# Kernel optimization log

Measured on AMD Instinct MI355X. Metric: run time of the kernel, lower is better.

The kernel has to match this reference:

```python
import jax, jax.numpy as jnp
import numpy as np

B, N, C = 4, 1024, 768
H, K, TEMP = 12, 32, 1.0
D = C // H
EPS = 1e-9


def setup_inputs() -> dict:
    key = jax.random.key(0)
    ks = jax.random.split(key, 5)
    x = jax.random.normal(ks[0], (B, N, C), dtype=jnp.float32)
    u = jax.random.uniform(ks[1], (B, N, N), dtype=jnp.float32)
    qkv_w = jax.random.normal(ks[2], (C, 3 * C), dtype=jnp.float32) * 0.02
    qkv_b = jnp.zeros((3 * C,), dtype=jnp.float32)
    proj_w = jax.random.normal(ks[3], (C, C), dtype=jnp.float32) * 0.02
    proj_b = jnp.zeros((C,), dtype=jnp.float32)
    head_scores = jnp.ones((H,), dtype=jnp.float32)
    return {"x": x, "u": u, "qkv_w": qkv_w, "qkv_b": qkv_b,
            "proj_w": proj_w, "proj_b": proj_b, "head_scores": head_scores}


def reference(x, u, qkv_w, qkv_b, proj_w, proj_b, head_scores):
    # qkv projection: [B,N,3C] -> [3,B,H,N,D]
    qkv = (x @ qkv_w + qkv_b).reshape(B, N, 3, H, D)
    qkv = jnp.transpose(qkv, (2, 0, 3, 1, 4))
    q, k, v = qkv[0], qkv[1], qkv[2]

    scale = 1.0 / np.sqrt(D)
    # full dense scores [B,H,N,N] (torch computes this twice; same math once)
    scores = jnp.einsum('bhnd,bhmd->bhnm', q, k) * scale

    # Gumbel top-K gate over head-averaged logits
    logits = scores.mean(axis=1)                         # [B,N,N]
    gumbel = -jnp.log(-jnp.log(u + EPS) + EPS)
    probs = jax.nn.softmax((logits + gumbel) / TEMP, axis=-1)
    topk_vals = jax.lax.top_k(probs, K)[0]               # sorted descending
    thresh = topk_vals[..., -1:]                          # K-th largest
    sparse_mask = (probs >= thresh).astype(scores.dtype)  # [B,N,N]

    # post-softmax masking (breaks flash fusion)
    attn = jax.nn.softmax(scores, axis=-1) * sparse_mask[:, None]
    out = jnp.einsum('bhnm,bhmd->bhnd', attn, v)          # [B,H,N,D]
    out = jnp.transpose(out, (0, 2, 1, 3)).reshape(B, N, C)
    return (out * head_scores.mean()) @ proj_w + proj_b
```

## Files before the change

kernel.cpp:

```cpp
#include <hip/hip_runtime.h>
#include <hip/hip_bf16.h>
#include <math.h>

#define B_ 4
#define N_ 1024
#define C_ 768
#define H_ 12
#define D_ 64
#define TOPK_ 32
#define EPS_ 1e-9f

#define LDN_ 32
#define LK_  72
#define QKS_ 1536

typedef __attribute__((ext_vector_type(8))) short bf16x8;
typedef __attribute__((ext_vector_type(4))) float f32x4;
typedef unsigned short u16;

struct TopkRec { unsigned int cnt; unsigned short c[62]; };

__device__ __forceinline__ u16 f2bf(float f) {
    unsigned int u = __float_as_uint(f);
    u += 0x7fffu + ((u >> 16) & 1u);
    return (u16)(u >> 16);
}
__device__ __forceinline__ float bf2f(u16 h) {
    return __uint_as_float(((unsigned int)h) << 16);
}

__device__ __forceinline__ void gll16(const void* g, void* l) {
    __builtin_amdgcn_global_load_lds(
        (const __attribute__((address_space(1))) void*)g,
        (__attribute__((address_space(3))) void*)l, 16, 0, 0);
}

__global__ __launch_bounds__(256) void conv_x(
    const float* __restrict__ X, u16* __restrict__ Xh, u16* __restrict__ Xl)
{
    const size_t off = ((size_t)blockIdx.x * 256 + threadIdx.x) * 8;
    float4 a = *(const float4*)&X[off];
    float4 b = *(const float4*)&X[off + 4];
    float v[8] = {a.x, a.y, a.z, a.w, b.x, b.y, b.z, b.w};
    u16 hb[8], lb[8];
    #pragma unroll
    for (int i = 0; i < 8; ++i) {
        u16 hi = f2bf(v[i]);
        hb[i] = hi;
        lb[i] = f2bf(v[i] - bf2f(hi));
    }
    *(bf16x8*)&Xh[off] = *(const bf16x8*)&hb[0];
    *(bf16x8*)&Xl[off] = *(const bf16x8*)&lb[0];
}

__global__ __launch_bounds__(256) void conv_w_nt(
    const float* __restrict__ W, u16* __restrict__ Wt_h, u16* __restrict__ Wt_l,
    int Kdim, int Ncols)
{
    __shared__ float Ts[64][65];
    const int t  = threadIdx.x;
    const int r  = t >> 2;
    const int cq = (t & 3) * 16;
    const int n0 = blockIdx.x * 64, k0 = blockIdx.y * 64;

    #pragma unroll
    for (int q = 0; q < 4; ++q) {
        float4 v = *(const float4*)&W[(size_t)(k0 + r) * Ncols + n0 + cq + q * 4];
        Ts[r][cq + q * 4 + 0] = v.x;
        Ts[r][cq + q * 4 + 1] = v.y;
        Ts[r][cq + q * 4 + 2] = v.z;
        Ts[r][cq + q * 4 + 3] = v.w;
    }
    __syncthreads();
    u16 hb[16], lb[16];
    #pragma unroll
    for (int i = 0; i < 16; ++i) {
        float val = Ts[cq + i][r];
        u16 hi = f2bf(val);
        hb[i] = hi;
        lb[i] = f2bf(val - bf2f(hi));
    }
    const size_t obase = (size_t)(n0 + r) * Kdim + k0 + cq;
    *(bf16x8*)&Wt_h[obase]     = *(const bf16x8*)&hb[0];
    *(bf16x8*)&Wt_h[obase + 8] = *(const bf16x8*)&hb[8];
    *(bf16x8*)&Wt_l[obase]     = *(const bf16x8*)&lb[0];
    *(bf16x8*)&Wt_l[obase + 8] = *(const bf16x8*)&lb[8];
}

__global__ __launch_bounds__(256) void gemm_qkv(
    const u16* __restrict__ Ath, const u16* __restrict__ Atl,
    const u16* __restrict__ Bth, const u16* __restrict__ Btl,
    const float* __restrict__ bias,
    u16* __restrict__ Ch, u16* __restrict__ Cl, float* __restrict__ Vf)
{
    __shared__ __align__(16) char smem[34816];
    u16* Ah = (u16*)(smem);
    u16* Al = (u16*)(smem + 8192);
    u16* Bh = (u16*)(smem + 16384);
    u16* Bl = (u16*)(smem + 24576);

    const int t    = threadIdx.x;
    const int d    = blockIdx.x;
    const int xcd  = d & 7, j = d >> 3;
    const int xt   = (xcd & 1) * 9 + (j % 9);
    const int yt   = (xcd >> 1) * 8 + (j / 9);
    const int m0   = yt * 128, n0 = xt * 128;
    const int lane = t & 63, w = t >> 6;
    const int wm   = (w >> 1) * 64, wn = (w & 1) * 64;
    const int fr   = lane & 15, kg8 = lane >> 4;
    const int w16  = w * 16;
    const int r4s  = lane >> 2, q4s = (lane & 3) * 8;

    f32x4 acc[4][4];
    #pragma unroll
    for (int i = 0; i < 4; ++i)
        #pragma unroll
        for (int j2 = 0; j2 < 4; ++j2)
            acc[i][j2] = (f32x4){0.f, 0.f, 0.f, 0.f};

    for (int kt = 0; kt < 24; ++kt) {
        const int k0 = kt * 32;
        __syncthreads();
        {
            const size_t ga0 = (size_t)(m0 + w16 + r4s) * C_ + k0 + q4s;
            const size_t ga1 = ga0 + (size_t)64 * C_;
            const size_t gb0 = (size_t)(n0 + w16 + r4s) * C_ + k0 + q4s;
            const size_t gb1 = gb0 + (size_t)64 * C_;
            gll16(&Ath[ga0], &Ah[w16 * LDN_]);
            gll16(&Ath[ga1], &Ah[(64 + w16) * LDN_]);
            gll16(&Atl[ga0], &Al[w16 * LDN_]);
            gll16(&Atl[ga1], &Al[(64 + w16) * LDN_]);
            gll16(&Bth[gb0], &Bh[w16 * LDN_]);
            gll16(&Bth[gb1], &Bh[(64 + w16) * LDN_]);
            gll16(&Btl[gb0], &Bl[w16 * LDN_]);
            gll16(&Btl[gb1], &Bl[(64 + w16) * LDN_]);
        }
        __syncthreads();

        bf16x8 aF[4], bF[4], a2F[4], b2F[4];
        #pragma unroll
        for (int fm = 0; fm < 4; ++fm)
            aF[fm] = *(const bf16x8*)&Ah[(wm + fm * 16 + fr) * LDN_ + kg8 * 8];
        #pragma unroll
        for (int fn = 0; fn < 4; ++fn)
            bF[fn] = *(const bf16x8*)&Bh[(wn + fn * 16 + fr) * LDN_ + kg8 * 8];
        #pragma unroll
        for (int fm = 0; fm < 4; ++fm)
            #pragma unroll
            for (int fn = 0; fn < 4; ++fn)
                acc[fm][fn] = __builtin_amdgcn_mfma_f32_16x16x32_bf16(
                    aF[fm], bF[fn], acc[fm][fn], 0, 0, 0);
        #pragma unroll
        for (int fn = 0; fn < 4; ++fn)
            b2F[fn] = *(const bf16x8*)&Bl[(wn + fn * 16 + fr) * LDN_ + kg8 * 8];
        #pragma unroll
        for (int fm = 0; fm < 4; ++fm)
            #pragma unroll
            for (int fn = 0; fn < 4; ++fn)
                acc[fm][fn] = __builtin_amdgcn_mfma_f32_16x16x32_bf16(
                    aF[fm], b2F[fn], acc[fm][fn], 0, 0, 0);
        #pragma unroll
        for (int fm = 0; fm < 4; ++fm)
            a2F[fm] = *(const bf16x8*)&Al[(wm + fm * 16 + fr) * LDN_ + kg8 * 8];
        #pragma unroll
        for (int fm = 0; fm < 4; ++fm)
            #pragma unroll
            for (int fn = 0; fn < 4; ++fn)
                acc[fm][fn] = __builtin_amdgcn_mfma_f32_16x16x32_bf16(
                    a2F[fm], bF[fn], acc[fm][fn], 0, 0, 0);
    }
    __syncthreads();

    const bool isV = (n0 >= 1536);
    float* Ts = (float*)(smem + w * 8448);
    const int lr8 = lane >> 3, lc8 = (lane & 7) * 8;
    #pragma unroll
    for (int p = 0; p < 2; ++p) {
        #pragma unroll
        for (int fmh = 0; fmh < 2; ++fmh) {
            const int fm = p * 2 + fmh;
            #pragma unroll
            for (int fn = 0; fn < 4; ++fn) {
                const float bv = bias[n0 + wn + fn * 16 + fr];
                #pragma unroll
                for (int i = 0; i < 4; ++i)
                    Ts[(fmh * 16 + kg8 * 4 + i) * 66 + fn * 16 + fr] =
                        acc[fm][fn][i] + bv;
            }
        }
        #pragma unroll
        for (int it = 0; it < 4; ++it) {
            const int r = it * 8 + lr8;
            float v[8];
            #pragma unroll
            for (int c = 0; c < 8; ++c) v[c] = Ts[r * 66 + lc8 + c];
            const int grow = m0 + wm + p * 32 + r;
            const int gcol = n0 + wn + lc8;
            if (isV) {
                float4 v0 = {v[0], v[1], v[2], v[3]};
                float4 v1 = {v[4], v[5], v[6], v[7]};
                float* vp = &Vf[(size_t)grow * C_ + gcol - 1536];
                *(float4*)vp       = v0;
                *(float4*)(vp + 4) = v1;
            } else {
                u16 hb[8], lb[8];
                #pragma unroll
                for (int c = 0; c < 8; ++c) {
                    u16 hi = f2bf(v[c]);
                    hb[c] = hi;
                    lb[c] = f2bf(v[c] - bf2f(hi));
                }
                *(bf16x8*)&Ch[(size_t)grow * QKS_ + gcol] = *(const bf16x8*)&hb[0];
                *(bf16x8*)&Cl[(size_t)grow * QKS_ + gcol] = *(const bf16x8*)&lb[0];
            }
        }
    }
}

__global__ __launch_bounds__(256) void attn_fused(
    const u16* __restrict__ qh, const u16* __restrict__ ql,
    const float* __restrict__ u, float* __restrict__ z,
    float2* __restrict__ mlp)
{
    __shared__ u16 KsH[128 * LK_], KsL[128 * LK_];

    const int t    = threadIdx.x;
    const int lane = t & 63, w = t >> 6;
    const int fr   = lane & 15, kg8 = lane >> 4;
    const int n0   = blockIdx.x * 64;
    const int m0   = blockIdx.y * 128;
    const int mc   = blockIdx.y;
    const int b    = blockIdx.z;

    f32x4 zacc[8];
    #pragma unroll
    for (int fn = 0; fn < 8; ++fn) zacc[fn] = (f32x4){0.f, 0.f, 0.f, 0.f};

    const int skr = t >> 1, skd = (t & 1) * 32;

    bf16x8 kAr[8], kBr[8], qAr[4], qBr[4];

    auto loadK = [&](bf16x8 (&kr)[8], int hd) {
        const size_t kb = (size_t)(b * N_ + m0 + skr) * QKS_ + 768 + hd * 64 + skd;
        kr[0] = *(const bf16x8*)&qh[kb];
        kr[1] = *(const bf16x8*)&qh[kb + 8];
        kr[2] = *(const bf16x8*)&qh[kb + 16];
        kr[3] = *(const bf16x8*)&qh[kb + 24];
        kr[4] = *(const bf16x8*)&ql[kb];
        kr[5] = *(const bf16x8*)&ql[kb + 8];
        kr[6] = *(const bf16x8*)&ql[kb + 16];
        kr[7] = *(const bf16x8*)&ql[kb + 24];
    };
    auto loadQ = [&](bf16x8 (&qr)[4], int hd) {
        const size_t qb = (size_t)(b * N_ + n0 + w * 16 + fr) * QKS_ + hd * 64 + kg8 * 8;
        qr[0] = *(const bf16x8*)&qh[qb];
        qr[1] = *(const bf16x8*)&qh[qb + 32];
        qr[2] = *(const bf16x8*)&ql[qb];
        qr[3] = *(const bf16x8*)&ql[qb + 32];
    };
    auto writeK = [&](const bf16x8 (&kr)[8]) {
        const int sb = skr * LK_ + skd;
        *(bf16x8*)&KsH[sb]      = kr[0];  *(bf16x8*)&KsH[sb + 8]  = kr[1];
        *(bf16x8*)&KsH[sb + 16] = kr[2];  *(bf16x8*)&KsH[sb + 24] = kr[3];
        *(bf16x8*)&KsL[sb]      = kr[4];  *(bf16x8*)&KsL[sb + 8]  = kr[5];
        *(bf16x8*)&KsL[sb + 16] = kr[6];  *(bf16x8*)&KsL[sb + 24] = kr[7];
    };
    auto compute = [&](const bf16x8 (&qr)[4], int hd) {
        f32x4 acc[8];
        #pragma unroll
        for (int fn = 0; fn < 8; ++fn) acc[fn] = (f32x4){0.f, 0.f, 0.f, 0.f};
        #pragma unroll
        for (int fn = 0; fn < 8; ++fn) {
            const int bidx = (fn * 16 + fr) * LK_ + kg8 * 8;
            bf16x8 bH = *(const bf16x8*)&KsH[bidx];
            bf16x8 bL = *(const bf16x8*)&KsL[bidx];
            acc[fn] = __builtin_amdgcn_mfma_f32_16x16x32_bf16(qr[0], bH, acc[fn], 0, 0, 0);
            acc[fn] = __builtin_amdgcn_mfma_f32_16x16x32_bf16(qr[0], bL, acc[fn], 0, 0, 0);
            acc[fn] = __builtin_amdgcn_mfma_f32_16x16x32_bf16(qr[2], bH, acc[fn], 0, 0, 0);
        }
        #pragma unroll
        for (int fn = 0; fn < 8; ++fn) {
            const int bidx = (fn * 16 + fr) * LK_ + 32 + kg8 * 8;
            bf16x8 bH = *(const bf16x8*)&KsH[bidx];
            bf16x8 bL = *(const bf16x8*)&KsL[bidx];
            acc[fn] = __builtin_amdgcn_mfma_f32_16x16x32_bf16(qr[1], bH, acc[fn], 0, 0, 0);
            acc[fn] = __builtin_amdgcn_mfma_f32_16x16x32_bf16(qr[1], bL, acc[fn], 0, 0, 0);
            acc[fn] = __builtin_amdgcn_mfma_f32_16x16x32_bf16(qr[3], bH, acc[fn], 0, 0, 0);
        }
        #pragma unroll
        for (int fn = 0; fn < 8; ++fn) {
            zacc[fn][0] += acc[fn][0];
            zacc[fn][1] += acc[fn][1];
            zacc[fn][2] += acc[fn][2];
            zacc[fn][3] += acc[fn][3];
        }
        #pragma unroll
        for (int reg = 0; reg < 4; ++reg) {
            float tmax = acc[0][reg];
            #pragma unroll
            for (int fn = 1; fn < 8; ++fn) tmax = fmaxf(tmax, acc[fn][reg]);
            tmax *= 0.125f;
            tmax = fmaxf(tmax, __shfl_xor(tmax, 1));
            tmax = fmaxf(tmax, __shfl_xor(tmax, 2));
            tmax = fmaxf(tmax, __shfl_xor(tmax, 4));
            tmax = fmaxf(tmax, __shfl_xor(tmax, 8));
            float tsum = 0.f;
            #pragma unroll
            for (int fn = 0; fn < 8; ++fn)
                tsum += expf(acc[fn][reg] * 0.125f - tmax);
            tsum += __shfl_xor(tsum, 1);
            tsum += __shfl_xor(tsum, 2);
            tsum += __shfl_xor(tsum, 4);
            tsum += __shfl_xor(tsum, 8);
            if (fr == 0) {
                const int n = n0 + w * 16 + kg8 * 4 + reg;
                mlp[(((size_t)(b * H_ + hd)) * N_ + n) * 8 + mc] =
                    make_float2(tmax, tsum);
            }
        }
    };

    loadQ(qAr, 0);
    loadK(kAr, 0);
    for (int hp = 0; hp < 6; ++hp) {
        const int hd0 = hp * 2, hd1 = hp * 2 + 1;
        __syncthreads();
        writeK(kAr);
        __syncthreads();
        loadQ(qBr, hd1);
        loadK(kBr, hd1);
        compute(qAr, hd0);
        __syncthreads();
        writeK(kBr);
        __syncthreads();
        if (hp < 5) {
            loadQ(qAr, hd0 + 2);
            loadK(kAr, hd0 + 2);
        }
        compute(qBr, hd1);
    }

    const float sc = 0.125f / 12.0f;
    #pragma unroll
    for (int fn = 0; fn < 8; ++fn) {
        const int m = m0 + fn * 16 + fr;
        #pragma unroll
        for (int reg = 0; reg < 4; ++reg) {
            const int n = n0 + w * 16 + kg8 * 4 + reg;
            const float uv = u[((size_t)(b * N_ + n)) * N_ + m];
            const float g  = -logf(-logf(uv + EPS_) + EPS_);
            z[((size_t)(b * N_ + n)) * N_ + m] = zacc[fn][reg] * sc + g;
        }
    }
}

__global__ __launch_bounds__(256) void ml_merge(
    const float2* __restrict__ mlp, float2* __restrict__ ml)
{
    const size_t idx = (size_t)blockIdx.x * 256 + threadIdx.x;
    float2 p[8];
    #pragma unroll
    for (int i = 0; i < 8; ++i) p[i] = mlp[idx * 8 + i];
    float m = p[0].x;
    #pragma unroll
    for (int i = 1; i < 8; ++i) m = fmaxf(m, p[i].x);
    float l = 0.f;
    #pragma unroll
    for (int i = 0; i < 8; ++i) l += p[i].y * expf(p[i].x - m);
    ml[idx] = make_float2(m, l);
}

__global__ __launch_bounds__(64) void topk_cols_kernel(
    const float* __restrict__ z, TopkRec* __restrict__ recs)
{
    const int row  = blockIdx.x;
    const int lane = threadIdx.x;
    const float* zr = z + (size_t)row * N_;
    float zv[16], wk[16];
    #pragma unroll
    for (int j = 0; j < 16; ++j) { zv[j] = zr[lane + 64 * j]; wk[j] = zv[j]; }

    float thresh = -INFINITY;
    for (int it = 0; it < TOPK_; ++it) {
        float lm = wk[0]; int li = 0;
        #pragma unroll
        for (int j = 1; j < 16; ++j)
            if (wk[j] > lm) { lm = wk[j]; li = j; }
        float gm = lm;
        gm = fmaxf(gm, __shfl_xor(gm, 1));
        gm = fmaxf(gm, __shfl_xor(gm, 2));
        gm = fmaxf(gm, __shfl_xor(gm, 4));
        gm = fmaxf(gm, __shfl_xor(gm, 8));
        gm = fmaxf(gm, __shfl_xor(gm, 16));
        gm = fmaxf(gm, __shfl_xor(gm, 32));
        unsigned long long has = __ballot(lm == gm);
        int first = __ffsll((unsigned long long)has) - 1;
        if (lane == first) wk[li] = -INFINITY;
        thresh = gm;
    }

    const unsigned long long below = ((unsigned long long)1 << lane) - 1;
    unsigned int basec = 0;
    TopkRec* rec = recs + row;
    #pragma unroll
    for (int j = 0; j < 16; ++j) {
        unsigned long long wmask = __ballot(zv[j] >= thresh);
        if (zv[j] >= thresh) {
            unsigned int pos = basec + (unsigned int)__popcll(wmask & below);
            if (pos < 62u) rec->c[pos] = (unsigned short)(lane + 64 * j);
        }
        basec += (unsigned int)__popcll(wmask);
    }
    if (lane == 0) rec->cnt = basec > 62u ? 62u : basec;
}

__global__ __launch_bounds__(256) void sparse_pv_kernel(
    const u16* __restrict__ qh, const u16* __restrict__ ql,
    const float* __restrict__ Vf,
    const TopkRec* __restrict__ recs, const float2* __restrict__ ml,
    const float* __restrict__ head_scores,
    u16* __restrict__ out1h, u16* __restrict__ out1l)
{
    __shared__ int cols_s[62];
    __shared__ int cnt_s;

    const int t    = threadIdx.x;
    const int lane = t & 63, wv = t >> 6;
    const int c4   = lane >> 2;
    const int dq   = lane & 3;
    const int row  = blockIdx.x;
    const int b    = row >> 10, n = row & 1023;

    const TopkRec* rec = recs + row;
    if (t == 0) cnt_s = (int)min(rec->cnt, 62u);
    if (t < 62) cols_s[t] = rec->c[t];

    float hsum = 0.f;
    #pragma unroll
    for (int i = 0; i < H_; ++i) hsum += head_scores[i];
    const float hs_mean = hsum * (1.0f / 12.0f);
    __syncthreads();
    const int cnt = cnt_s;
    const int nbatch = (cnt + 15) >> 4;

    for (int hd = wv; hd < H_; hd += 4) {
        float qv[16];
        {
            const size_t qb = (size_t)row * QKS_ + hd * 64 + dq * 16;
            bf16x8 qh0 = *(const bf16x8*)&qh[qb], qh1 = *(const bf16x8*)&qh[qb + 8];
            bf16x8 ql0 = *(const bf16x8*)&ql[qb], ql1 = *(const bf16x8*)&ql[qb + 8];
            #pragma unroll
            for (int i = 0; i < 8; ++i) {
                qv[i]     = bf2f((u16)qh0[i]) + bf2f((u16)ql0[i]);
                qv[i + 8] = bf2f((u16)qh1[i]) + bf2f((u16)ql1[i]);
            }
        }
        const float2 mlv = ml[((size_t)(b * H_ + hd)) * N_ + n];

        float acc[16];
        #pragma unroll
        for (int i = 0; i < 16; ++i) acc[i] = 0.f;

        for (int batch = 0; batch < nbatch; ++batch) {
            const int cidx  = batch * 16 + c4;
            const bool valid = (cidx < cnt);
            const int col   = cols_s[valid ? cidx : cnt - 1];

            const size_t kb = (size_t)(b * N_ + col) * QKS_ + 768 + hd * 64 + dq * 16;
            bf16x8 kh0 = *(const bf16x8*)&qh[kb], kh1 = *(const bf16x8*)&qh[kb + 8];
            bf16x8 kl0 = *(const bf16x8*)&ql[kb], kl1 = *(const bf16x8*)&ql[kb + 8];
            float dot = 0.f;
            #pragma unroll
            for (int i = 0; i < 8; ++i) {
                dot += qv[i]     * (bf2f((u16)kh0[i]) + bf2f((u16)kl0[i]));
                dot += qv[i + 8] * (bf2f((u16)kh1[i]) + bf2f((u16)kl1[i]));
            }
            dot += __shfl_xor(dot, 1);
            dot += __shfl_xor(dot, 2);
            float p = valid ? expf(dot * 0.125f - mlv.x) : 0.f;

            const float* vb = &Vf[(size_t)(b * N_ + col) * C_ + hd * 64 + dq * 16];
            #pragma unroll
            for (int q = 0; q < 4; ++q) {
                float4 v4 = *(const float4*)&vb[q * 4];
                acc[q * 4 + 0] += p * v4.x;
                acc[q * 4 + 1] += p * v4.y;
                acc[q * 4 + 2] += p * v4.z;
                acc[q * 4 + 3] += p * v4.w;
            }
        }

        #pragma unroll
        for (int d = 4; d < 64; d <<= 1)
            #pragma unroll
            for (int i = 0; i < 16; ++i)
                acc[i] += __shfl_xor(acc[i], d);

        if (c4 == 0) {
            const float s = hs_mean / mlv.y;
            u16 hb[16], lb[16];
            #pragma unroll
            for (int i = 0; i < 16; ++i) {
                float val = acc[i] * s;
                u16 hi = f2bf(val);
                hb[i] = hi;
                lb[i] = f2bf(val - bf2f(hi));
            }
            const size_t ob = (size_t)row * C_ + hd * 64 + dq * 16;
            *(bf16x8*)&out1h[ob]     = *(const bf16x8*)&hb[0];
            *(bf16x8*)&out1h[ob + 8] = *(const bf16x8*)&hb[8];
            *(bf16x8*)&out1l[ob]     = *(const bf16x8*)&lb[0];
            *(bf16x8*)&out1l[ob + 8] = *(const bf16x8*)&lb[8];
        }
    }
}

__global__ __launch_bounds__(256) void gemm_proj(
    const u16* __restrict__ Ath, const u16* __restrict__ Atl,
    const u16* __restrict__ Bth, const u16* __restrict__ Btl,
    const float* __restrict__ bias, float* __restrict__ Cm)
{
    __shared__ __align__(16) char smem[33792];
    u16* Ah = (u16*)(smem);
    u16* Al = (u16*)(smem + 4096);
    u16* Bh = (u16*)(smem + 8192);
    u16* Bl = (u16*)(smem + 16384);

    const int t    = threadIdx.x;
    const int d    = blockIdx.x;
    const int xcd  = d & 7, j = d >> 3;
    const int xt   = j % 6;
    const int yt   = xcd * 8 + j / 6;
    const int m0   = yt * 64, n0 = xt * 128;
    const int lane = t & 63, w = t >> 6;
    const int wm   = (w & 1) * 32, wn = (w >> 1) * 64;
    const int fr   = lane & 15, kg8 = lane >> 4;
    const int w16  = w * 16;
    const int r4s  = lane >> 2, q4s = (lane & 3) * 8;

    f32x4 acc[2][4];
    #pragma unroll
    for (int i = 0; i < 2; ++i)
        #pragma unroll
        for (int j2 = 0; j2 < 4; ++j2)
            acc[i][j2] = (f32x4){0.f, 0.f, 0.f, 0.f};

    for (int kt = 0; kt < 24; ++kt) {
        const int k0 = kt * 32;
        __syncthreads();
        {
            const size_t ga  = (size_t)(m0 + w16 + r4s) * C_ + k0 + q4s;
            const size_t gb0 = (size_t)(n0 + w * 32 + r4s) * C_ + k0 + q4s;
            const size_t gb1 = gb0 + (size_t)16 * C_;
            gll16(&Ath[ga],  &Ah[w16 * LDN_]);
            gll16(&Atl[ga],  &Al[w16 * LDN_]);
            gll16(&Bth[gb0], &Bh[(w * 32) * LDN_]);
            gll16(&Bth[gb1], &Bh[(w * 32 + 16) * LDN_]);
            gll16(&Btl[gb0], &Bl[(w * 32) * LDN_]);
            gll16(&Btl[gb1], &Bl[(w * 32 + 16) * LDN_]);
        }
        __syncthreads();

        bf16x8 aF[2], bF[4], a2F[2], b2F[4];
        #pragma unroll
        for (int fm = 0; fm < 2; ++fm)
            aF[fm] = *(const bf16x8*)&Ah[(wm + fm * 16 + fr) * LDN_ + kg8 * 8];
        #pragma unroll
        for (int fn = 0; fn < 4; ++fn)
            bF[fn] = *(const bf16x8*)&Bh[(wn + fn * 16 + fr) * LDN_ + kg8 * 8];
        #pragma unroll
        for (int fm = 0; fm < 2; ++fm)
            #pragma unroll
            for (int fn = 0; fn < 4; ++fn)
                acc[fm][fn] = __builtin_amdgcn_mfma_f32_16x16x32_bf16(
                    aF[fm], bF[fn], acc[fm][fn], 0, 0, 0);
        #pragma unroll
        for (int fn = 0; fn < 4; ++fn)
            b2F[fn] = *(const bf16x8*)&Bl[(wn + fn * 16 + fr) * LDN_ + kg8 * 8];
        #pragma unroll
        for (int fm = 0; fm < 2; ++fm)
            #pragma unroll
            for (int fn = 0; fn < 4; ++fn)
                acc[fm][fn] = __builtin_amdgcn_mfma_f32_16x16x32_bf16(
                    aF[fm], b2F[fn], acc[fm][fn], 0, 0, 0);
        #pragma unroll
        for (int fm = 0; fm < 2; ++fm)
            a2F[fm] = *(const bf16x8*)&Al[(wm + fm * 16 + fr) * LDN_ + kg8 * 8];
        #pragma unroll
        for (int fm = 0; fm < 2; ++fm)
            #pragma unroll
            for (int fn = 0; fn < 4; ++fn)
                acc[fm][fn] = __builtin_amdgcn_mfma_f32_16x16x32_bf16(
                    a2F[fm], bF[fn], acc[fm][fn], 0, 0, 0);
    }
    __syncthreads();

    float* Ts = (float*)(smem + w * 8448);
    const int lr8 = lane >> 3, lc8 = (lane & 7) * 8;
    #pragma unroll
    for (int fm = 0; fm < 2; ++fm)
        #pragma unroll
        for (int fn = 0; fn < 4; ++fn) {
            const float bv = bias[n0 + wn + fn * 16 + fr];
            #pragma unroll
            for (int i = 0; i < 4; ++i)
                Ts[(fm * 16 + kg8 * 4 + i) * 66 + fn * 16 + fr] =
                    acc[fm][fn][i] + bv;
        }
    #pragma unroll
    for (int it = 0; it < 4; ++it) {
        const int r = it * 8 + lr8;
        float v[8];
        #pragma unroll
        for (int c = 0; c < 8; ++c) v[c] = Ts[r * 66 + lc8 + c];
        const int grow = m0 + wm + r;
        const int gcol = n0 + wn + lc8;
        float4 v0 = {v[0], v[1], v[2], v[3]};
        float4 v1 = {v[4], v[5], v[6], v[7]};
        float* cp = &Cm[(size_t)grow * C_ + gcol];
        *(float4*)cp       = v0;
        *(float4*)(cp + 4) = v1;
    }
}

extern "C" void kernel_launch(void* const* d_in, const int* in_sizes, int n_in,
                              void* d_out, int out_size, void* d_ws, size_t ws_size,
                              hipStream_t stream)
{
    (void)in_sizes; (void)n_in; (void)out_size; (void)ws_size;
    const float* x           = (const float*)d_in[0];
    const float* u           = (const float*)d_in[1];
    const float* qkv_w       = (const float*)d_in[2];
    const float* qkv_b       = (const float*)d_in[3];
    const float* proj_w      = (const float*)d_in[4];
    const float* proj_b      = (const float*)d_in[5];
    const float* head_scores = (const float*)d_in[6];
    float* out = (float*)d_out;

    char* ws = (char*)d_ws;
    u16*     qkv_h  = (u16*)ws;
    u16*     qkv_l  = (u16*)(ws + 12582912);
    float*   Vf     = (float*)(ws + 25165824);
    char*    R      = ws + 37748736;
    u16*     wq_t_h = (u16*)R;
    u16*     wq_t_l = (u16*)(R + 3538944);
    float*   z      = (float*)R;
    TopkRec* recs   = (TopkRec*)(R + 16777216);
    u16*     wp_t_h = (u16*)R;
    u16*     wp_t_l = (u16*)(R + 1179648);
    float2*  ml     = (float2*)(R + 2359296);
    u16*     out1h  = (u16*)(R + 2752512);
    u16*     out1l  = (u16*)(R + 9043968);
    u16*     x_h    = (u16*)d_out;
    u16*     x_l    = (u16*)((char*)d_out + 6291456);
    float2*  mlp    = (float2*)d_out;

    conv_x<<<dim3(4096 * 768 / 8 / 256), dim3(256), 0, stream>>>(x, x_h, x_l);

    conv_w_nt<<<dim3(2304 / 64, 768 / 64), dim3(256), 0, stream>>>(
        qkv_w, wq_t_h, wq_t_l, 768, 2304);

    gemm_qkv<<<dim3(576), dim3(256), 0, stream>>>(
        x_h, x_l, wq_t_h, wq_t_l, qkv_b, qkv_h, qkv_l, Vf);

    attn_fused<<<dim3(16, 8, B_), dim3(256), 0, stream>>>(
        qkv_h, qkv_l, u, z, mlp);

    topk_cols_kernel<<<dim3(B_ * N_), dim3(64), 0, stream>>>(z, recs);

    conv_w_nt<<<dim3(768 / 64, 768 / 64), dim3(256), 0, stream>>>(
        proj_w, wp_t_h, wp_t_l, 768, 768);

    ml_merge<<<dim3(B_ * H_ * N_ / 256), dim3(256), 0, stream>>>(mlp, ml);

    sparse_pv_kernel<<<dim3(B_ * N_), dim3(256), 0, stream>>>(
        qkv_h, qkv_l, Vf, recs, ml, head_scores, out1h, out1l);

    gemm_proj<<<dim3(384), dim3(256), 0, stream>>>(
        out1h, out1l, wp_t_h, wp_t_l, proj_b, out);
}
```

Before: 269.5 us.

## Double-buffer LDS tiles in QKV and projection GEMMs to overlap loads

Both split-bf16 GEMM kernels now use two LDS buffers and prefetch the next K-tile with global-to-LDS loads while the current tile feeds the MFMAs. Partial vmcnt waits and raw barriers replace the two __syncthreads per iteration, so global latency is meant to be hidden behind compute. LDS use roughly doubles (64KB and 48KB per block), which can lower occupancy.

```diff
diff --git a/kernel.cpp b/kernel.cpp
--- a/kernel.cpp
+++ b/kernel.cpp
@@ -93,11 +93,7 @@
     const float* __restrict__ bias,
     u16* __restrict__ Ch, u16* __restrict__ Cl, float* __restrict__ Vf)
 {
-    __shared__ __align__(16) char smem[34816];
-    u16* Ah = (u16*)(smem);
-    u16* Al = (u16*)(smem + 8192);
-    u16* Bh = (u16*)(smem + 16384);
-    u16* Bl = (u16*)(smem + 24576);
+    __shared__ __align__(16) char smem[65536];
 
     const int t    = threadIdx.x;
     const int d    = blockIdx.x;
@@ -111,6 +107,26 @@
     const int w16  = w * 16;
     const int r4s  = lane >> 2, q4s = (lane & 3) * 8;
 
+    auto stage = [&](int k0, int buf) {
+        char* base = smem + buf * 32768;
+        u16* Ah = (u16*)(base);
+        u16* Al = (u16*)(base + 8192);
+        u16* Bh = (u16*)(base + 16384);
+        u16* Bl = (u16*)(base + 24576);
+        const size_t ga0 = (size_t)(m0 + w16 + r4s) * C_ + k0 + q4s;
+        const size_t ga1 = ga0 + (size_t)64 * C_;
+        const size_t gb0 = (size_t)(n0 + w16 + r4s) * C_ + k0 + q4s;
+        const size_t gb1 = gb0 + (size_t)64 * C_;
+        gll16(&Ath[ga0], &Ah[w16 * LDN_]);
+        gll16(&Ath[ga1], &Ah[(64 + w16) * LDN_]);
+        gll16(&Atl[ga0], &Al[w16 * LDN_]);
+        gll16(&Atl[ga1], &Al[(64 + w16) * LDN_]);
+        gll16(&Bth[gb0], &Bh[w16 * LDN_]);
+        gll16(&Bth[gb1], &Bh[(64 + w16) * LDN_]);
+        gll16(&Btl[gb0], &Bl[w16 * LDN_]);
+        gll16(&Btl[gb1], &Bl[(64 + w16) * LDN_]);
+    };
+
     f32x4 acc[4][4];
     #pragma unroll
     for (int i = 0; i < 4; ++i)
@@ -118,24 +134,25 @@
         for (int j2 = 0; j2 < 4; ++j2)
             acc[i][j2] = (f32x4){0.f, 0.f, 0.f, 0.f};
 
+    stage(0, 0);
     for (int kt = 0; kt < 24; ++kt) {
-        const int k0 = kt * 32;
-        __syncthreads();
-        {
-            const size_t ga0 = (size_t)(m0 + w16 + r4s) * C_ + k0 + q4s;
-            const size_t ga1 = ga0 + (size_t)64 * C_;
-            const size_t gb0 = (size_t)(n0 + w16 + r4s) * C_ + k0 + q4s;
-            const size_t gb1 = gb0 + (size_t)64 * C_;
-            gll16(&Ath[ga0], &Ah[w16 * LDN_]);
-            gll16(&Ath[ga1], &Ah[(64 + w16) * LDN_]);
-            gll16(&Atl[ga0], &Al[w16 * LDN_]);
-            gll16(&Atl[ga1], &Al[(64 + w16) * LDN_]);
-            gll16(&Bth[gb0], &Bh[w16 * LDN_]);
-            gll16(&Bth[gb1], &Bh[(64 + w16) * LDN_]);
-            gll16(&Btl[gb0], &Bl[w16 * LDN_]);
-            gll16(&Btl[gb1], &Bl[(64 + w16) * LDN_]);
-        }
-        __syncthreads();
+        if (kt < 23) {
+            asm volatile("s_waitcnt lgkmcnt(0)" ::: "memory");
+            __builtin_amdgcn_s_barrier();
+            __builtin_amdgcn_sched_barrier(0);
+            stage((kt + 1) * 32, (kt + 1) & 1);
+            asm volatile("s_waitcnt vmcnt(8)" ::: "memory");
+        } else {
+            asm volatile("s_waitcnt vmcnt(0)" ::: "memory");
+        }
+        __builtin_amdgcn_s_barrier();
+        __builtin_amdgcn_sched_barrier(0);
+
+        char* base = smem + (kt & 1) * 32768;
+        u16* Ah = (u16*)(base);
+        u16* Al = (u16*)(base + 8192);
+        u16* Bh = (u16*)(base + 16384);
+        u16* Bl = (u16*)(base + 24576);
 
         bf16x8 aF[4], bF[4], a2F[4], b2F[4];
         #pragma unroll
@@ -520,11 +537,7 @@
     const u16* __restrict__ Bth, const u16* __restrict__ Btl,
     const float* __restrict__ bias, float* __restrict__ Cm)
 {
-    __shared__ __align__(16) char smem[33792];
-    u16* Ah = (u16*)(smem);
-    u16* Al = (u16*)(smem + 4096);
-    u16* Bh = (u16*)(smem + 8192);
-    u16* Bl = (u16*)(smem + 16384);
+    __shared__ __align__(16) char smem[49152];
 
     const int t    = threadIdx.x;
     const int d    = blockIdx.x;
@@ -538,6 +551,23 @@
     const int w16  = w * 16;
     const int r4s  = lane >> 2, q4s = (lane & 3) * 8;
 
+    auto stage = [&](int k0, int buf) {
+        char* base = smem + buf * 24576;
+        u16* Ah = (u16*)(base);
+        u16* Al = (u16*)(base + 4096);
+        u16* Bh = (u16*)(base + 8192);
+        u16* Bl = (u16*)(base + 16384);
+        const size_t ga  = (size_t)(m0 + w16 + r4s) * C_ + k0 + q4s;
+        const size_t gb0 = (size_t)(n0 + w * 32 + r4s) * C_ + k0 + q4s;
+        const size_t gb1 = gb0 + (size_t)16 * C_;
+        gll16(&Ath[ga],  &Ah[w16 * LDN_]);
+        gll16(&Atl[ga],  &Al[w16 * LDN_]);
+        gll16(&Bth[gb0], &Bh[(w * 32) * LDN_]);
+        gll16(&Bth[gb1], &Bh[(w * 32 + 16) * LDN_]);
+        gll16(&Btl[gb0], &Bl[(w * 32) * LDN_]);
+        gll16(&Btl[gb1], &Bl[(w * 32 + 16) * LDN_]);
+    };
+
     f32x4 acc[2][4];
     #pragma unroll
     for (int i = 0; i < 2; ++i)
@@ -545,21 +575,25 @@
         for (int j2 = 0; j2 < 4; ++j2)
             acc[i][j2] = (f32x4){0.f, 0.f, 0.f, 0.f};
 
+    stage(0, 0);
     for (int kt = 0; kt < 24; ++kt) {
-        const int k0 = kt * 32;
-        __syncthreads();
-        {
-            const size_t ga  = (size_t)(m0 + w16 + r4s) * C_ + k0 + q4s;
-            const size_t gb0 = (size_t)(n0 + w * 32 + r4s) * C_ + k0 + q4s;
-            const size_t gb1 = gb0 + (size_t)16 * C_;
-            gll16(&Ath[ga],  &Ah[w16 * LDN_]);
-            gll16(&Atl[ga],  &Al[w16 * LDN_]);
-            gll16(&Bth[gb0], &Bh[(w * 32) * LDN_]);
-            gll16(&Bth[gb1], &Bh[(w * 32 + 16) * LDN_]);
-            gll16(&Btl[gb0], &Bl[(w * 32) * LDN_]);
-            gll16(&Btl[gb1], &Bl[(w * 32 + 16) * LDN_]);
-        }
-        __syncthreads();
+        if (kt < 23) {
+            asm volatile("s_waitcnt lgkmcnt(0)" ::: "memory");
+            __builtin_amdgcn_s_barrier();
+            __builtin_amdgcn_sched_barrier(0);
+            stage((kt + 1) * 32, (kt + 1) & 1);
+            asm volatile("s_waitcnt vmcnt(6)" ::: "memory");
+        } else {
+            asm volatile("s_waitcnt vmcnt(0)" ::: "memory");
+        }
+        __builtin_amdgcn_s_barrier();
+        __builtin_amdgcn_sched_barrier(0);
+
+        char* base = smem + (kt & 1) * 24576;
+        u16* Ah = (u16*)(base);
+        u16* Al = (u16*)(base + 4096);
+        u16* Bh = (u16*)(base + 8192);
+        u16* Bl = (u16*)(base + 16384);
 
         bf16x8 aF[2], bF[4], a2F[2], b2F[4];
         #pragma unroll
```

After: 260.8 us. 3.2% less time.
